# Kernel optimization log

Hardware: AMD Instinct MI355X
Metric: run time of the kernel (lower is better)

Reference implementation:

```python
import jax, jax.numpy as jnp
import numpy as np

B, NI, NO = 4, 256, 256          # batch, num_in, num_out
DIN, DQ, DH, DOUT = 256, 256, 256, 256


def setup_inputs() -> dict:
    key = jax.random.key(0)
    ks = jax.random.split(key, 6)
    def w(k, shape, fan_in):
        return jax.random.normal(k, shape, jnp.float32) / np.sqrt(fan_in).astype(np.float32)
    return {
        "x": jax.random.normal(ks[0], (B, NI, DIN), jnp.float32),
        "query": jax.random.normal(ks[1], (B, NO, DQ), jnp.float32),
        # pre_cond_mlp: Linear(DIN -> DH)
        "W_pre": w(ks[2], (DIN, DH), DIN), "b_pre": jnp.zeros((DH,), jnp.float32),
        # cond_embed: Linear(DQ -> DH)
        "W_emb": w(ks[3], (DQ, DH), DQ), "b_emb": jnp.zeros((DH,), jnp.float32),
        # post_cond_mlp: Linear(2*DH -> DH) + GELU + Linear(DH -> DOUT)
        "W1": w(ks[4], (2 * DH, DH), 2 * DH), "b1": jnp.zeros((DH,), jnp.float32),
        "W2": w(ks[5], (DH, DOUT), DH), "b2": jnp.zeros((DOUT,), jnp.float32),
    }


def reference(x, query, W_pre, b_pre, W_emb, b_emb, W1, b1, W2, b2):
    # pre_cond_mlp(x): [B, NI, DH]
    xp = x @ W_pre + b_pre
    # cond_embed(query): [B, NO, DH]
    c = query @ W_emb + b_emb
    # Original torch code: repeat xp over NO, c over NI, concat -> [B,NI,NO,2*DH],
    # then Linear(2*DH->DH). Algebraically identical (and far cheaper) to split W1
    # and broadcast-add the two projections:
    W1x, W1c = W1[:DH], W1[DH:]          # [DH, DH] each
    h = (xp @ W1x)[:, :, None, :] + (c @ W1c)[:, None, :, :] + b1  # [B, NI, NO, DH]
    h = jax.nn.gelu(h, approximate=False)  # torch nn.GELU default = exact erf
    return h @ W2 + b2                     # [B, NI, NO, DOUT]
```

## Files before the change

kernel.cpp:

```cpp
#include <hip/hip_runtime.h>
#include <hip/hip_bf16.h>
#include <cstdint>
#include <cstddef>


typedef __bf16  bf16x8 __attribute__((ext_vector_type(8)));
typedef float   f32x16 __attribute__((ext_vector_type(16)));

__device__ __forceinline__ float fast_gelu(float x) {
    const float x2 = x * x;
    const float m  = __builtin_fmaf(x2, -0.1029433f, -2.3022072f);
    const float e  = __builtin_amdgcn_exp2f(x * m);
    return x * __builtin_amdgcn_rcpf(1.0f + e);
}

__global__ __launch_bounds__(256) void prep_kernel(
    const float* __restrict__ x, const float* __restrict__ query,
    const float* __restrict__ W_pre, const float* __restrict__ b_pre,
    const float* __restrict__ W_emb, const float* __restrict__ b_emb,
    const float* __restrict__ W1, const float* __restrict__ b1,
    const float* __restrict__ W2,
    float* __restrict__ u, float* __restrict__ v,
    unsigned short* __restrict__ w2f)
{
    const int b = blockIdx.x;
    const int t = threadIdx.x;

    if (b >= 512) {
        const int n0 = (b - 512) * 4;
        const float4 wv = *reinterpret_cast<const float4*>(W2 + (size_t)t * 256 + n0);
        const float vals[4] = {wv.x, wv.y, wv.z, wv.w};
        const int g = t >> 3, e = t & 7;
#pragma unroll
        for (int j = 0; j < 4; ++j) {
            const __bf16 bv = (__bf16)vals[j];
            w2f[((size_t)(g * 256 + n0 + j)) * 8 + e] =
                __builtin_bit_cast(unsigned short, bv);
        }
        return;
    }

    const bool isq = (b >= 256);
    const float* __restrict__ A   = isq ? query : x;
    const float* __restrict__ Wa  = isq ? W_emb : W_pre;
    const float* __restrict__ ba  = isq ? b_emb : b_pre;
    const float* __restrict__ W1p = isq ? (W1 + 256 * 256) : W1;
    float* __restrict__ outp      = isq ? v : u;
    const int r0 = (isq ? (b - 256) : b) * 4;

    __shared__ float as[4][256];
    __shared__ float xs[4][256];

#pragma unroll
    for (int r = 0; r < 4; ++r)
        as[r][t] = A[(size_t)(r0 + r) * 256 + t];
    __syncthreads();

    float acc[4] = {0.f, 0.f, 0.f, 0.f};
    {
        float wcur[8];
#pragma unroll
        for (int q = 0; q < 8; ++q) wcur[q] = Wa[(size_t)q * 256 + t];
        for (int k0 = 0; k0 < 248; k0 += 8) {
            float wnxt[8];
#pragma unroll
            for (int q = 0; q < 8; ++q)
                wnxt[q] = Wa[(size_t)(k0 + 8 + q) * 256 + t];
#pragma unroll
            for (int q = 0; q < 8; ++q)
#pragma unroll
                for (int r = 0; r < 4; ++r)
                    acc[r] = __builtin_fmaf(as[r][k0 + q], wcur[q], acc[r]);
#pragma unroll
            for (int q = 0; q < 8; ++q) wcur[q] = wnxt[q];
        }
#pragma unroll
        for (int q = 0; q < 8; ++q)
#pragma unroll
            for (int r = 0; r < 4; ++r)
                acc[r] = __builtin_fmaf(as[r][248 + q], wcur[q], acc[r]);
    }
    const float bav = ba[t];
#pragma unroll
    for (int r = 0; r < 4; ++r) xs[r][t] = acc[r] + bav;
    __syncthreads();

    float acc2[4] = {0.f, 0.f, 0.f, 0.f};
    {
        float wcur[8];
#pragma unroll
        for (int q = 0; q < 8; ++q) wcur[q] = W1p[(size_t)q * 256 + t];
        for (int k0 = 0; k0 < 248; k0 += 8) {
            float wnxt[8];
#pragma unroll
            for (int q = 0; q < 8; ++q)
                wnxt[q] = W1p[(size_t)(k0 + 8 + q) * 256 + t];
#pragma unroll
            for (int q = 0; q < 8; ++q)
#pragma unroll
                for (int r = 0; r < 4; ++r)
                    acc2[r] = __builtin_fmaf(xs[r][k0 + q], wcur[q], acc2[r]);
#pragma unroll
            for (int q = 0; q < 8; ++q) wcur[q] = wnxt[q];
        }
#pragma unroll
        for (int q = 0; q < 8; ++q)
#pragma unroll
            for (int r = 0; r < 4; ++r)
                acc2[r] = __builtin_fmaf(xs[r][248 + q], wcur[q], acc2[r]);
    }
    const float b1v = isq ? 0.f : b1[t];
#pragma unroll
    for (int r = 0; r < 4; ++r)
        outp[(size_t)(r0 + r) * 256 + t] = acc2[r] + b1v;
}

__global__ __launch_bounds__(256, 3) void fused_kernel(
    const float* __restrict__ U, const float* __restrict__ V,
    const unsigned short* __restrict__ W2F, const float* __restrict__ b2,
    float* __restrict__ out)
{
    __shared__ uint4 hlds[1024];
    __shared__ uint4 blds[2][1024];
    unsigned int* const h32 = reinterpret_cast<unsigned int*>(hlds);

    const int t    = threadIdx.x;
    const int lane = t & 63;
    const int w    = t >> 6;
    const int l31  = lane & 31;
    const int hi   = lane >> 5;

    const int bid  = blockIdx.x;
    const int tile = bid >> 1;
    const int jh   = bid & 1;
    const int bb   = tile >> 8;

    const float* __restrict__ urow  = U + (size_t)tile * 256;
    const float* __restrict__ vbase = V + ((size_t)(bb * 256 + jh * 128)) * 256;

    const int d  = t & 31;
    const int rb = t >> 5;

    auto stage_b = [&](int cg, int buf) {
#pragma unroll
        for (int it = 0; it < 4; ++it) {
            const int idx = it * 256 + t;
            const int g   = idx >> 5;
            const int c   = idx & 31;
            __builtin_amdgcn_global_load_lds(
                (const __attribute__((address_space(1))) unsigned int*)
                    (W2F + ((size_t)(g * 256 + cg * 32 + c)) * 8),
                (__attribute__((address_space(3))) unsigned int*)
                    (&blds[buf][idx]),
                16, 0, 0);
        }
    };

    stage_b(0, 0);

    bf16x8 af[16];
#pragma unroll
    for (int c = 0; c < 4; ++c) {
        const int kk = c * 64;
        const float2 u2 = *reinterpret_cast<const float2*>(urow + kk + 2 * d);
        float2 vv[16];
#pragma unroll
        for (int p = 0; p < 16; ++p) {
            const int row = rb + p * 8;
            vv[p] = *reinterpret_cast<const float2*>(
                vbase + (size_t)row * 256 + kk + 2 * d);
        }
#pragma unroll
        for (int p = 0; p < 16; ++p) {
            const int row = rb + p * 8;
            union { unsigned int u32; __bf16 h[2]; } pk;
            pk.h[0] = (__bf16)fast_gelu(u2.x + vv[p].x);
            pk.h[1] = (__bf16)fast_gelu(u2.y + vv[p].y);
            h32[row * 32 + (((d >> 2) ^ (row & 7)) << 2) + (d & 3)] = pk.u32;
        }
        __syncthreads();
        const int arow = w * 32 + l31;
#pragma unroll
        for (int s = 0; s < 4; ++s) {
            const int gl = 2 * s + hi;
            af[c * 4 + s] = __builtin_bit_cast(
                bf16x8, hlds[arow * 8 + (gl ^ (arow & 7))]);
        }
        __syncthreads();
    }

    float bvv[8];
#pragma unroll
    for (int cg = 0; cg < 8; ++cg) bvv[cg] = b2[cg * 32 + l31];

    const size_t obase = ((size_t)tile << 16) + (size_t)(jh * 128 + w * 32) * 256;

#pragma unroll
    for (int cg = 0; cg < 8; ++cg) {
        if (cg < 7) stage_b(cg + 1, (cg + 1) & 1);

        f32x16 acc = (f32x16)0.f;
#pragma unroll
        for (int S = 0; S < 16; ++S) {
            const bf16x8 bf_ = __builtin_bit_cast(
                bf16x8, blds[cg & 1][(2 * S + hi) * 32 + l31]);
            acc = __builtin_amdgcn_mfma_f32_32x32x16_bf16(af[S], bf_, acc, 0, 0, 0);
        }

        __syncthreads();

        const int col = cg * 32 + l31;
#pragma unroll
        for (int rr = 0; rr < 16; ++rr) {
            const int row = 4 * hi + (rr & 3) + 8 * (rr >> 2);
            out[obase + (size_t)row * 256 + col] = acc[rr] + bvv[cg];
        }
    }
}

extern "C" void kernel_launch(void* const* d_in, const int* in_sizes, int n_in,
                              void* d_out, int out_size, void* d_ws, size_t ws_size,
                              hipStream_t stream)
{
    const float* x     = (const float*)d_in[0];
    const float* query = (const float*)d_in[1];
    const float* W_pre = (const float*)d_in[2];
    const float* b_pre = (const float*)d_in[3];
    const float* W_emb = (const float*)d_in[4];
    const float* b_emb = (const float*)d_in[5];
    const float* W1    = (const float*)d_in[6];
    const float* b1    = (const float*)d_in[7];
    const float* W2    = (const float*)d_in[8];
    const float* b2    = (const float*)d_in[9];
    float* out = (float*)d_out;

    char* ws = (char*)d_ws;
    float* u            = (float*)(ws);
    float* v            = (float*)(ws + (1 << 20));
    unsigned short* w2f = (unsigned short*)(ws + 2 * (1 << 20));

    prep_kernel<<<576, 256, 0, stream>>>(x, query, W_pre, b_pre, W_emb, b_emb,
                                         W1, b1, W2, u, v, w2f);
    fused_kernel<<<2048, 256, 0, stream>>>(u, v, w2f, b2, out);
}
```

Measured before the change: 91.75 us.

## Process both row halves per block, overlapping GELU staging with first-half MFMAs

Each block now handles a whole 256-row tile instead of half of it, so the grid is halved. The GELU/bf16 staging of the second half's A fragments is interleaved with the MFMA passes and output stores of the first half, and the W2 tile staging continues across both halves. The goal is to hide the elementwise producer phase behind matrix work and cut per-block setup. In exchange, two A fragment sets stay live at once, which raises register pressure, so occupancy is lowered to 2 blocks per SIMD group.

New measurement: 105.5 us. 1.15x slower.

```diff
diff --git a/kernel.cpp b/kernel.cpp
--- a/kernel.cpp
+++ b/kernel.cpp
@@ -115,7 +115,7 @@
         outp[(size_t)(r0 + r) * 256 + t] = acc2[r] + b1v;
 }
 
-__global__ __launch_bounds__(256, 3) void fused_kernel(
+__global__ __launch_bounds__(256, 2) void fused_kernel(
     const float* __restrict__ U, const float* __restrict__ V,
     const unsigned short* __restrict__ W2F, const float* __restrict__ b2,
     float* __restrict__ out)
@@ -130,16 +130,16 @@
     const int l31  = lane & 31;
     const int hi   = lane >> 5;
 
-    const int bid  = blockIdx.x;
-    const int tile = bid >> 1;
-    const int jh   = bid & 1;
+    const int tile = blockIdx.x;
     const int bb   = tile >> 8;
 
-    const float* __restrict__ urow  = U + (size_t)tile * 256;
-    const float* __restrict__ vbase = V + ((size_t)(bb * 256 + jh * 128)) * 256;
+    const float* __restrict__ urow   = U + (size_t)tile * 256;
+    const float* __restrict__ vbaseA = V + ((size_t)(bb * 256)) * 256;
+    const float* __restrict__ vbaseB = V + ((size_t)(bb * 256 + 128)) * 256;
 
     const int d  = t & 31;
     const int rb = t >> 5;
+    const int arow = w * 32 + l31;
 
     auto stage_b = [&](int cg, int buf) {
 #pragma unroll
@@ -156,11 +156,7 @@
         }
     };
 
-    stage_b(0, 0);
-
-    bf16x8 af[16];
-#pragma unroll
-    for (int c = 0; c < 4; ++c) {
+    auto p1_chunk_write = [&](const float* vbase, int c) {
         const int kk = c * 64;
         const float2 u2 = *reinterpret_cast<const float2*>(urow + kk + 2 * d);
         float2 vv[16];
@@ -178,12 +174,19 @@
             pk.h[1] = (__bf16)fast_gelu(u2.y + vv[p].y);
             h32[row * 32 + (((d >> 2) ^ (row & 7)) << 2) + (d & 3)] = pk.u32;
         }
-        __syncthreads();
-        const int arow = w * 32 + l31;
+    };
+
+    stage_b(0, 0);
+
+    bf16x8 afA[16];
+#pragma unroll
+    for (int c = 0; c < 4; ++c) {
+        p1_chunk_write(vbaseA, c);
+        __syncthreads();
 #pragma unroll
         for (int s = 0; s < 4; ++s) {
             const int gl = 2 * s + hi;
-            af[c * 4 + s] = __builtin_bit_cast(
+            afA[c * 4 + s] = __builtin_bit_cast(
                 bf16x8, hlds[arow * 8 + (gl ^ (arow & 7))]);
         }
         __syncthreads();
@@ -193,7 +196,56 @@
 #pragma unroll
     for (int cg = 0; cg < 8; ++cg) bvv[cg] = b2[cg * 32 + l31];
 
-    const size_t obase = ((size_t)tile << 16) + (size_t)(jh * 128 + w * 32) * 256;
+    const size_t obaseA = ((size_t)tile << 16) + (size_t)(w * 32) * 256;
+    const size_t obaseB = ((size_t)tile << 16) + (size_t)(128 + w * 32) * 256;
+
+    bf16x8 afB[16];
+#pragma unroll
+    for (int c = 0; c < 4; ++c) {
+        {
+            const int cg = 2 * c;
+            stage_b(cg + 1, (cg + 1) & 1);
+            f32x16 acc = (f32x16)0.f;
+#pragma unroll
+            for (int S = 0; S < 16; ++S) {
+                const bf16x8 bf_ = __builtin_bit_cast(
+                    bf16x8, blds[cg & 1][(2 * S + hi) * 32 + l31]);
+                acc = __builtin_amdgcn_mfma_f32_32x32x16_bf16(afA[S], bf_, acc, 0, 0, 0);
+            }
+            const int col = cg * 32 + l31;
+#pragma unroll
+            for (int rr = 0; rr < 16; ++rr) {
+                const int row = 4 * hi + (rr & 3) + 8 * (rr >> 2);
+                out[obaseA + (size_t)row * 256 + col] = acc[rr] + bvv[cg];
+            }
+        }
+        p1_chunk_write(vbaseB, c);
+        __syncthreads();
+        {
+            const int cg = 2 * c + 1;
+            stage_b((2 * c + 2) & 7, (2 * c + 2) & 1);
+            f32x16 acc = (f32x16)0.f;
+#pragma unroll
+            for (int S = 0; S < 16; ++S) {
+                const bf16x8 bf_ = __builtin_bit_cast(
+                    bf16x8, blds[cg & 1][(2 * S + hi) * 32 + l31]);
+                acc = __builtin_amdgcn_mfma_f32_32x32x16_bf16(afA[S], bf_, acc, 0, 0, 0);
+            }
+            const int col = cg * 32 + l31;
+#pragma unroll
+            for (int rr = 0; rr < 16; ++rr) {
+                const int row = 4 * hi + (rr & 3) + 8 * (rr >> 2);
+                out[obaseA + (size_t)row * 256 + col] = acc[rr] + bvv[cg];
+            }
+        }
+#pragma unroll
+        for (int s = 0; s < 4; ++s) {
+            const int gl = 2 * s + hi;
+            afB[c * 4 + s] = __builtin_bit_cast(
+                bf16x8, hlds[arow * 8 + (gl ^ (arow & 7))]);
+        }
+        __syncthreads();
+    }
 
 #pragma unroll
     for (int cg = 0; cg < 8; ++cg) {
@@ -204,17 +256,16 @@
         for (int S = 0; S < 16; ++S) {
             const bf16x8 bf_ = __builtin_bit_cast(
                 bf16x8, blds[cg & 1][(2 * S + hi) * 32 + l31]);
-            acc = __builtin_amdgcn_mfma_f32_32x32x16_bf16(af[S], bf_, acc, 0, 0, 0);
-        }
-
-        __syncthreads();
+            acc = __builtin_amdgcn_mfma_f32_32x32x16_bf16(afB[S], bf_, acc, 0, 0, 0);
+        }
 
         const int col = cg * 32 + l31;
 #pragma unroll
         for (int rr = 0; rr < 16; ++rr) {
             const int row = 4 * hi + (rr & 3) + 8 * (rr >> 2);
-            out[obase + (size_t)row * 256 + col] = acc[rr] + bvv[cg];
-        }
+            out[obaseB + (size_t)row * 256 + col] = acc[rr] + bvv[cg];
+        }
+        __syncthreads();
     }
 }
 
@@ -241,5 +292,5 @@
 
     prep_kernel<<<576, 256, 0, stream>>>(x, query, W_pre, b_pre, W_emb, b_emb,
                                          W1, b1, W2, u, v, w2f);
-    fused_kernel<<<2048, 256, 0, stream>>>(u, v, w2f, b2, out);
-}
+    fused_kernel<<<1024, 256, 0, stream>>>(u, v, w2f, b2, out);
+}
```
